# Kernel tuning notes

Hardware: AMD Instinct MI355X
Metric: run time of the kernel (lower is better)

Reference implementation:

```python
import jax, jax.numpy as jnp
import numpy as np
import math

H = 128      # hidden_channels
R = 32       # num_rbf
N = 4096     # atoms
E = 65536    # edges
CU = 4.5     # cutoff_upper (cutoff_lower = 0)
ALPHA = 5.0 / CU
MEANS = jnp.linspace(math.exp(-CU), 1.0, R, dtype=jnp.float32)
BETA = jnp.float32((2.0 / R * (1.0 - math.exp(-CU))) ** -2)
EPS = 1e-5


def _ln(x, g, b):
    mu = x.mean(-1, keepdims=True)
    var = ((x - mu) ** 2).mean(-1, keepdims=True)
    return (x - mu) * jax.lax.rsqrt(var + EPS) * g + b


def setup_inputs() -> dict:
    key = jax.random.key(0)
    ks = jax.random.split(key, 20)
    f32 = jnp.float32

    def w(i, shape):
        return jax.random.normal(ks[i], shape, f32) / np.float32(np.sqrt(shape[-1]))

    return {
        "edge_vec": jax.random.normal(ks[0], (E, 3), f32) * 1.5,
        "emb_w": w(1, (128, H)),
        "emb2_w": w(2, (H, 2 * H)), "emb2_b": jnp.zeros((H,), f32),
        "dp1_w": w(3, (H, R)), "dp1_b": jnp.zeros((H,), f32),
        "dp2_w": w(4, (H, R)), "dp2_b": jnp.zeros((H,), f32),
        "dp3_w": w(5, (H, R)), "dp3_b": jnp.zeros((H,), f32),
        "lt0_w": w(6, (H, H)), "lt1_w": w(7, (H, H)), "lt2_w": w(8, (H, H)),
        "ls0_w": w(9, (2 * H, H)), "ls0_b": jnp.zeros((2 * H,), f32),
        "ls1_w": w(10, (3 * H, 2 * H)), "ls1_b": jnp.zeros((3 * H,), f32),
        "init_g": jnp.ones((H,), f32), "init_b": jnp.zeros((H,), f32),
        "lin_w": w(11, (H, 3 * H)), "lin_b": jnp.zeros((H,), f32),
        "outn_g": jnp.ones((3 * H,), f32), "outn_b": jnp.zeros((3 * H,), f32),
        "ol1_w": w(12, (H // 2, H)), "ol1_b": jnp.zeros((H // 2,), f32),
        "ol2_w": w(13, (1, H // 2)), "ol2_b": jnp.zeros((1,), f32),
        "z": jax.random.randint(ks[14], (N,), 0, 128, dtype=jnp.int32),
        "edge_index": jax.random.randint(ks[15], (2, E), 0, N, dtype=jnp.int32),
    }


def reference(edge_vec, emb_w, emb2_w, emb2_b, dp1_w, dp1_b, dp2_w, dp2_b,
              dp3_w, dp3_b, lt0_w, lt1_w, lt2_w, ls0_w, ls0_b, ls1_w, ls1_b,
              init_g, init_b, lin_w, lin_b, outn_g, outn_b, ol1_w, ol1_b,
              ol2_w, ol2_b, z, edge_index):
    n = z.shape[0]
    src, dst = edge_index[0], edge_index[1]

    d = jnp.sqrt((edge_vec ** 2).sum(-1))                 # (E,)
    vn = edge_vec / d[:, None]                             # unit edge vectors
    cut = jnp.where(d < CU, 0.5 * (jnp.cos(jnp.pi * d / CU) + 1.0), 0.0)
    # expnorm RBF
    rbf = cut[:, None] * jnp.exp(-BETA * (jnp.exp(-ALPHA * d)[:, None] - MEANS) ** 2)  # (E,R)

    # atomic-number message Zij = emb2(cat(emb(z_i), emb(z_j)))
    zpair = jnp.concatenate([emb_w[z[src]], emb_w[z[dst]]], -1)  # (E,2H)
    zij = zpair @ emb2_w.T + emb2_b                              # (E,H)
    c = cut[:, None] * zij                                       # cutoff * Zij, (E,H)

    w1 = (rbf @ dp1_w.T + dp1_b) * c    # scalar channel weights (E,H)
    w2 = (rbf @ dp2_w.T + dp2_b) * c
    w3 = (rbf @ dp3_w.T + dp3_b) * c

    eye = jnp.eye(3, dtype=edge_vec.dtype)
    zero = jnp.zeros_like(vn[:, 0])
    skew = jnp.stack([zero, -vn[:, 2], vn[:, 1],
                      vn[:, 2], zero, -vn[:, 0],
                      -vn[:, 1], vn[:, 0], zero], 1).reshape(-1, 3, 3)  # (E,3,3)
    outer = vn[:, :, None] * vn[:, None, :]
    sym = outer - ((vn ** 2).sum(-1) / 3.0)[:, None, None] * eye        # traceless sym (E,3,3)

    seg = lambda a: jax.ops.segment_sum(a, src, num_segments=n)
    I0 = seg(w1)[:, :, None, None] * eye                                # (N,H,3,3)
    A0 = seg(w2[:, :, None, None] * skew[:, None, :, :])                # (N,H,3,3)
    S0 = seg(w3[:, :, None, None] * sym[:, None, :, :])                 # (N,H,3,3)

    tn = ((I0 + A0 + S0) ** 2).sum((-2, -1))                            # tensor_norm, (N,H)
    nrm = _ln(tn, init_g, init_b)
    h = jax.nn.silu(nrm @ ls0_w.T + ls0_b)
    scal = jax.nn.silu(h @ ls1_w.T + ls1_b).reshape(n, H, 3)            # per-channel gates

    I1 = jnp.einsum('nhxy,gh->ngxy', I0, lt0_w) * scal[..., 0][..., None, None]
    A1 = jnp.einsum('nhxy,gh->ngxy', A0, lt1_w) * scal[..., 1][..., None, None]
    S1 = jnp.einsum('nhxy,gh->ngxy', S0, lt2_w) * scal[..., 2][..., None, None]

    x = jnp.concatenate([(I1 ** 2).sum((-2, -1)),
                         (A1 ** 2).sum((-2, -1)),
                         (S1 ** 2).sum((-2, -1))], -1)                  # (N,3H)
    x = _ln(x, outn_g, outn_b)
    s1 = x @ lin_w.T + lin_b
    s2 = jax.nn.silu(s1) @ ol1_w.T + ol1_b
    s3 = jax.nn.silu(s2) @ ol2_w.T + ol2_b                              # per-atom energy (N,1)
    return s3
```

## Files before the change

kernel.cpp:

```cpp
#include <hip/hip_runtime.h>
#include <math.h>

#define NH_TOT 524288
#define N_ATOM 4096
#define N_EDGE 65536

typedef __attribute__((ext_vector_type(8))) short bf16x8;
typedef __attribute__((ext_vector_type(4))) float f32x4;

__device__ __forceinline__ unsigned short f2bf(float f) {
    unsigned u = __builtin_bit_cast(unsigned, f);
    unsigned r = (u + 0x7fffu + ((u >> 16) & 1u)) >> 16;
    return (unsigned short)r;
}
__device__ __forceinline__ float bf2f(unsigned short s) {
    unsigned u = ((unsigned)s) << 16;
    return __builtin_bit_cast(float, u);
}
__device__ __forceinline__ float silu(float v) { return v / (1.0f + __expf(-v)); }

#define WB_LS1 32768
#define WB_LT0 131072
#define WB_LT1 147456
#define WB_LT2 163840
#define WB_DP  180224

__global__ __launch_bounds__(256) void k_setup(
    const float* __restrict__ emb_w, const float* __restrict__ emb2_w,
    const int* __restrict__ ei, const int* __restrict__ z,
    const float* __restrict__ ls0_w, const float* __restrict__ ls1_w,
    const float* __restrict__ lt0_w, const float* __restrict__ lt1_w,
    const float* __restrict__ lt2_w,
    const float* __restrict__ dp1_w, const float* __restrict__ dp2_w,
    const float* __restrict__ dp3_w,
    float* __restrict__ U1, float* __restrict__ U2,
    int* __restrict__ cursor, int* __restrict__ order_pad,
    unsigned short* __restrict__ wb) {
    const int bx = blockIdx.x, tid = threadIdx.x;
    if (bx < 4096) {
        const int idx = bx * 4 + (tid >> 6);
        const int t = idx >> 7, h = idx & 127;
        const int lane = tid & 63;
        const float e0 = emb_w[t * 128 + lane];
        const float e1 = emb_w[t * 128 + 64 + lane];
        const float* row = emb2_w + h * 256;
        const float w0 = row[lane], w1 = row[64 + lane];
        const float w2 = row[128 + lane], w3 = row[192 + lane];
        float u1 = e0 * w0 + e1 * w1;
        float u2 = e0 * w2 + e1 * w3;
#pragma unroll
        for (int o = 1; o < 64; o <<= 1) {
            u1 += __shfl_xor(u1, o, 64);
            u2 += __shfl_xor(u2, o, 64);
        }
        if (lane == 0) {
            U1[t * 128 + h] = u1;
            U2[t * 128 + h] = u2;
        }
    } else if (bx < 4352) {
        const int e = (bx - 4096) * 256 + tid;
        const int src = ei[e];
        const int zd = z[ei[N_EDGE + e]];
        const int pos = atomicAdd(&cursor[src], 1);
        if (pos < 64) order_pad[(src << 6) + pos] = e | (zd << 16);
    } else {
        const int base = (bx - 4352) * 1024 + tid * 4;
        const float* src;
        int off;
        if (base < 32768)       { src = ls0_w; off = 0; }
        else if (base < 131072) { src = ls1_w; off = 32768; }
        else if (base < 147456) { src = lt0_w; off = 131072; }
        else if (base < 163840) { src = lt1_w; off = 147456; }
        else if (base < 180224) { src = lt2_w; off = 163840; }
        else if (base < 184320) { src = dp1_w; off = 180224; }
        else if (base < 188416) { src = dp2_w; off = 184320; }
        else                    { src = dp3_w; off = 188416; }
        const float4 v = *(const float4*)(src + (base - off));
        unsigned short* o = wb + base;
        o[0] = f2bf(v.x); o[1] = f2bf(v.y); o[2] = f2bf(v.z); o[3] = f2bf(v.w);
    }
}

__global__ __launch_bounds__(256) void k_fused(
    const int* __restrict__ z, const int* __restrict__ ecnt,
    const int* __restrict__ order_pad,
    const float* __restrict__ edge_vec,
    const float* __restrict__ U1, const float* __restrict__ U2,
    const float* __restrict__ emb2_b,
    const float* __restrict__ dp1_b, const float* __restrict__ dp2_b,
    const float* __restrict__ dp3_b,
    const unsigned short* __restrict__ wb,
    const float* __restrict__ init_g, const float* __restrict__ init_b,
    const float* __restrict__ ls0_b, const float* __restrict__ ls1_b,
    const float* __restrict__ outn_g, const float* __restrict__ outn_b,
    const float* __restrict__ lin_w, const float* __restrict__ lin_b,
    const float* __restrict__ ol1_w, const float* __restrict__ ol1_b,
    const float* __restrict__ ol2_w, const float* __restrict__ ol2_b,
    float* __restrict__ out) {
    const int tid = threadIdx.x;
    const int wave = tid >> 6, lane = tid & 63, lm = lane & 15, lq = lane >> 4;
    const int n0 = blockIdx.x * 8;
    const int ar = (lm < 8) ? lm : 7;

    __shared__ alignas(16) char smem[38912];
    unsigned short (*accs)[8][136] = reinterpret_cast<unsigned short(*)[8][136]>(smem);
    unsigned short (*nrms)[136]    = reinterpret_cast<unsigned short(*)[136]>(smem + 21760);
    unsigned short (*h1)[264]      = reinterpret_cast<unsigned short(*)[264]>(smem + 23936);
    unsigned short (*scal_s)[392]  = reinterpret_cast<unsigned short(*)[392]>(smem + 32384);
    float (*redS)[4]               = reinterpret_cast<float(*)[4]>(smem + 38656);
    float (*redQ)[4]               = reinterpret_cast<float(*)[4]>(smem + 38784);
    float (*xs)[392]               = reinterpret_cast<float(*)[392]>(smem);
    float (*ss)[132]               = reinterpret_cast<float(*)[132]>(smem + 23936);

    const unsigned short* dpw = wb + WB_DP;
    bf16x8 bfr[3][2];
    float bhc[2], bk1[2], bk2[2], bk3[2];
    int cols[2];
#pragma unroll
    for (int t = 0; t < 2; t++) {
        const int col = wave * 32 + t * 16 + lm;
        cols[t] = col;
        bhc[t] = emb2_b[col];
        bk1[t] = dp1_b[col]; bk2[t] = dp2_b[col]; bk3[t] = dp3_b[col];
#pragma unroll
        for (int k = 0; k < 3; k++)
            bfr[k][t] = *(const bf16x8*)(dpw + k * 4096 + col * 32 + lq * 8);
    }

    const float m0 = 0.011108996538242306f;
    const float dm = (1.0f - m0) * (1.0f / 31.0f);
    const float tb = 0.0625f * (1.0f - m0);
    const float beta = 1.0f / (tb * tb);
    const float mean0 = m0 + (float)(lq * 8) * dm;

    float tnA[8], tnB[8];

    for (int nn = 0; nn < 8; nn++) {
        const int n = n0 + nn;
        const int En = min(ecnt[n], 64);
        const int beg = n << 6;
        const int zoff = z[n] << 7;
        const float u1c0 = U1[zoff + cols[0]];
        const float u1c1 = U1[zoff + cols[1]];

        float part[10][2];
#pragma unroll
        for (int p = 0; p < 10; p++) { part[p][0] = 0.f; part[p][1] = 0.f; }

        for (int mi = 0; mi < En; mi += 16) {
            const int wrd = order_pad[beg + min(mi + lm, En - 1)];
            const int e = wrd & 0xFFFF;
            const int u2o = (wrd >> 16) << 7;
            const float evx = edge_vec[3 * e + 0];
            const float evy = edge_vec[3 * e + 1];
            const float evz = edge_vec[3 * e + 2];
            const float d = sqrtf(evx * evx + evy * evy + evz * evz);
            const float inv = 1.0f / d;
            const float cut = (d < 4.5f) ? 0.5f * (__cosf(0.6981317007977318f * d) + 1.0f) : 0.0f;
            const float vx = evx * inv, vy = evy * inv, vz = evz * inv;
            const float expd = __expf(-1.1111111111111112f * d);

            union { bf16x8 v; unsigned short s[8]; } uf;
#pragma unroll
            for (int j = 0; j < 8; j++) {
                const float df = expd - (mean0 + (float)j * dm);
                uf.s[j] = f2bf(cut * __expf(-beta * df * df));
            }
            const bf16x8 af = uf.v;

            f32x4 c[3][2];
#pragma unroll
            for (int k = 0; k < 3; k++)
#pragma unroll
                for (int t = 0; t < 2; t++)
                    c[k][t] = __builtin_amdgcn_mfma_f32_16x16x32_bf16(
                        af, bfr[k][t], (f32x4){0.f, 0.f, 0.f, 0.f}, 0, 0, 0);

#pragma unroll
            for (int r = 0; r < 4; r++) {
                const int er = mi + lq * 4 + r;
                const bool valid = er < En;
                const int sl = (lane & 48) | (lq * 4 + r);
                const float gvx = __shfl(vx, sl, 64);
                const float gvy = __shfl(vy, sl, 64);
                const float gvz = __shfl(vz, sl, 64);
                const float gct = __shfl(cut, sl, 64);
                const int   go  = __shfl(u2o, sl, 64);
#pragma unroll
                for (int t = 0; t < 2; t++) {
                    const float u2v = U2[go + cols[t]];
                    const float u1h = (t == 0) ? u1c0 : u1c1;
                    const float cc = valid ? gct * (u1h + u2v + bhc[t]) : 0.f;
                    const float w1 = (c[0][t][r] + bk1[t]) * cc;
                    const float w2 = (c[1][t][r] + bk2[t]) * cc;
                    const float w3 = (c[2][t][r] + bk3[t]) * cc;
                    part[0][t] += w1;
                    part[1][t] += w2 * gvx; part[2][t] += w2 * gvy; part[3][t] += w2 * gvz;
                    const float tx = w3 * gvx, ty = w3 * gvy;
                    part[4][t] += tx * gvx; part[5][t] += tx * gvy; part[6][t] += tx * gvz;
                    part[7][t] += ty * gvy; part[8][t] += ty * gvz; part[9][t] += w3 * gvz * gvz;
                }
            }
        }

#pragma unroll
        for (int p = 0; p < 10; p++)
#pragma unroll
            for (int t = 0; t < 2; t++) {
                float v = part[p][t];
                v += __shfl_xor(v, 16, 64);
                v += __shfl_xor(v, 32, 64);
                part[p][t] = v;
            }
        if (lq == 0) {
#pragma unroll
            for (int p = 0; p < 10; p++)
#pragma unroll
                for (int t = 0; t < 2; t++)
                    accs[p][nn][cols[t]] = f2bf(part[p][t]);
        }

        float tn[2];
#pragma unroll
        for (int t = 0; t < 2; t++) {
            const float aI = part[0][t];
            const float axv = part[1][t], ayv = part[2][t], azv = part[3][t];
            const float mxx = part[4][t], mxy = part[5][t], mxz = part[6][t];
            const float myy = part[7][t], myz = part[8][t], mzz = part[9][t];
            const float tr3 = (mxx + myy + mzz) * (1.0f / 3.0f);
            const float t00 = aI + mxx - tr3;
            const float t11 = aI + myy - tr3;
            const float t22 = aI + mzz - tr3;
            tn[t] = t00 * t00 + t11 * t11 + t22 * t22 +
                    2.0f * (mxy * mxy + azv * azv + mxz * mxz + ayv * ayv + myz * myz + axv * axv);
        }
        tnA[nn] = tn[0];
        tnB[nn] = tn[1];

        float s = (lq == 0) ? (tn[0] + tn[1]) : 0.f;
        s += __shfl_xor(s, 1, 64);
        s += __shfl_xor(s, 2, 64);
        s += __shfl_xor(s, 4, 64);
        s += __shfl_xor(s, 8, 64);
        if (lane == 0) redS[nn][wave] = s;
    }
    __syncthreads();

    {
        float dvA[8], dvB[8];
#pragma unroll
        for (int nn = 0; nn < 8; nn++) {
            const float mu = (redS[nn][0] + redS[nn][1] + redS[nn][2] + redS[nn][3]) * (1.0f / 128.0f);
            dvA[nn] = tnA[nn] - mu;
            dvB[nn] = tnB[nn] - mu;
            float q = (lq == 0) ? (dvA[nn] * dvA[nn] + dvB[nn] * dvB[nn]) : 0.f;
            q += __shfl_xor(q, 1, 64);
            q += __shfl_xor(q, 2, 64);
            q += __shfl_xor(q, 4, 64);
            q += __shfl_xor(q, 8, 64);
            if (lane == 0) redQ[nn][wave] = q;
        }
        __syncthreads();
        if (lq == 0) {
            const float g0 = init_g[cols[0]], g1 = init_g[cols[1]];
            const float b0 = init_b[cols[0]], b1 = init_b[cols[1]];
#pragma unroll
            for (int nn = 0; nn < 8; nn++) {
                const float var = (redQ[nn][0] + redQ[nn][1] + redQ[nn][2] + redQ[nn][3]) * (1.0f / 128.0f);
                const float rs = rsqrtf(var + 1e-5f);
                nrms[nn][cols[0]] = f2bf(dvA[nn] * rs * g0 + b0);
                nrms[nn][cols[1]] = f2bf(dvB[nn] * rs * g1 + b1);
            }
        }
    }
    __syncthreads();

    {
        f32x4 acc[4];
#pragma unroll
        for (int j = 0; j < 4; j++) acc[j] = (f32x4){0.f, 0.f, 0.f, 0.f};
        const int cbase = wave * 64;
#pragma unroll
        for (int kc = 0; kc < 128; kc += 32) {
            const bf16x8 af = *(const bf16x8*)(&nrms[ar][kc + lq * 8]);
#pragma unroll
            for (int sn = 0; sn < 4; sn++) {
                const bf16x8 b = *(const bf16x8*)(wb + (size_t)(cbase + sn * 16 + lm) * 128 + kc + lq * 8);
                acc[sn] = __builtin_amdgcn_mfma_f32_16x16x32_bf16(af, b, acc[sn], 0, 0, 0);
            }
        }
#pragma unroll
        for (int sn = 0; sn < 4; sn++) {
            const int col = cbase + sn * 16 + lm;
            const float bv = ls0_b[col];
#pragma unroll
            for (int r = 0; r < 4; r++)
                h1[lq * 4 + r][col] = f2bf(silu(acc[sn][r] + bv));
        }
    }
    __syncthreads();
    {
        f32x4 acc[6];
#pragma unroll
        for (int j = 0; j < 6; j++) acc[j] = (f32x4){0.f, 0.f, 0.f, 0.f};
        const int cbase = wave * 96;
        const unsigned short* ls1p = wb + WB_LS1;
#pragma unroll 2
        for (int kc = 0; kc < 256; kc += 32) {
            const bf16x8 af = *(const bf16x8*)(&h1[lm][kc + lq * 8]);
#pragma unroll
            for (int sn = 0; sn < 6; sn++) {
                const bf16x8 b = *(const bf16x8*)(ls1p + (size_t)(cbase + sn * 16 + lm) * 256 + kc + lq * 8);
                acc[sn] = __builtin_amdgcn_mfma_f32_16x16x32_bf16(af, b, acc[sn], 0, 0, 0);
            }
        }
#pragma unroll
        for (int sn = 0; sn < 6; sn++) {
            const int col = cbase + sn * 16 + lm;
            const float bv = ls1_b[col];
#pragma unroll
            for (int r = 0; r < 4; r++) {
                const int node = lq * 4 + r;
                if (node < 8) scal_s[node][col] = f2bf(silu(acc[sn][r] + bv));
            }
        }
    }
    __syncthreads();

    f32x4 e0[2], e1[2], e2[2], trv[2];
#pragma unroll
    for (int sn = 0; sn < 2; sn++) {
        e0[sn] = (f32x4){0.f, 0.f, 0.f, 0.f};
        e1[sn] = (f32x4){0.f, 0.f, 0.f, 0.f};
        e2[sn] = (f32x4){0.f, 0.f, 0.f, 0.f};
        trv[sn] = (f32x4){0.f, 0.f, 0.f, 0.f};
    }
#pragma unroll
    for (int p = 0; p < 10; p++) {
        const unsigned short* B = wb + (p == 0 ? WB_LT0 : (p < 4 ? WB_LT1 : WB_LT2));
        f32x4 c[2];
        c[0] = (f32x4){0.f, 0.f, 0.f, 0.f};
        c[1] = (f32x4){0.f, 0.f, 0.f, 0.f};
#pragma unroll
        for (int kc = 0; kc < 128; kc += 32) {
            const bf16x8 af = *(const bf16x8*)(&accs[p][ar][kc + lq * 8]);
#pragma unroll
            for (int sn = 0; sn < 2; sn++) {
                const bf16x8 b = *(const bf16x8*)(B + (size_t)(wave * 32 + sn * 16 + lm) * 128 + kc + lq * 8);
                c[sn] = __builtin_amdgcn_mfma_f32_16x16x32_bf16(af, b, c[sn], 0, 0, 0);
            }
        }
#pragma unroll
        for (int sn = 0; sn < 2; sn++) {
            if (p == 0)      e0[sn] += c[sn] * c[sn];
            else if (p < 4)  e1[sn] += c[sn] * c[sn];
            else if (p == 4 || p == 7 || p == 9) { e2[sn] += c[sn] * c[sn]; trv[sn] += c[sn]; }
            else             e2[sn] += 2.0f * c[sn] * c[sn];
        }
    }
    __syncthreads();

    if (lq < 2) {
#pragma unroll
        for (int sn = 0; sn < 2; sn++) {
            const int g = wave * 32 + sn * 16 + lm;
#pragma unroll
            for (int r = 0; r < 4; r++) {
                const int node = lq * 4 + r;
                const float s0 = bf2f(scal_s[node][3 * g + 0]);
                const float s1 = bf2f(scal_s[node][3 * g + 1]);
                const float s2 = bf2f(scal_s[node][3 * g + 2]);
                xs[node][g]       = 3.0f * e0[sn][r] * s0 * s0;
                xs[node][128 + g] = 2.0f * e1[sn][r] * s1 * s1;
                const float tr = trv[sn][r];
                xs[node][256 + g] = (e2[sn][r] - tr * tr * (1.0f / 3.0f)) * s2 * s2;
            }
        }
    }
    __syncthreads();

#pragma unroll
    for (int i = 0; i < 2; i++) {
        const int node = wave * 2 + i;
        float v[6];
        float s = 0.f;
#pragma unroll
        for (int j = 0; j < 6; j++) { v[j] = xs[node][lane + 64 * j]; s += v[j]; }
#pragma unroll
        for (int o = 1; o < 64; o <<= 1) s += __shfl_xor(s, o, 64);
        const float mu = s * (1.0f / 384.0f);
        float q = 0.f;
#pragma unroll
        for (int j = 0; j < 6; j++) { v[j] -= mu; q += v[j] * v[j]; }
#pragma unroll
        for (int o = 1; o < 64; o <<= 1) q += __shfl_xor(q, o, 64);
        const float rs = rsqrtf(q * (1.0f / 384.0f) + 1e-5f);
#pragma unroll
        for (int j = 0; j < 6; j++) {
            const int col = lane + 64 * j;
            xs[node][col] = v[j] * rs * outn_g[col] + outn_b[col];
        }
    }
    __syncthreads();

    {
        const int j = tid & 127, half = tid >> 7;
        float a4[4];
        const float lb = lin_b[j];
#pragma unroll
        for (int i = 0; i < 4; i++) a4[i] = lb;
        const float4* wr = (const float4*)(lin_w + j * 384);
#pragma unroll 2
        for (int k4 = 0; k4 < 96; k4++) {
            const float4 w4 = wr[k4];
#pragma unroll
            for (int i = 0; i < 4; i++) {
                const float4 xv = *(const float4*)&xs[half * 4 + i][k4 * 4];
                a4[i] += w4.x * xv.x + w4.y * xv.y + w4.z * xv.z + w4.w * xv.w;
            }
        }
        __syncthreads();
#pragma unroll
        for (int i = 0; i < 4; i++) ss[half * 4 + i][j] = silu(a4[i]);
    }
    __syncthreads();

    {
        const int o = tid & 63, q = tid >> 6;
        float a2v[2];
        const float ob = ol1_b[o];
        a2v[0] = ob; a2v[1] = ob;
        const float4* o4 = (const float4*)(ol1_w + o * 128);
#pragma unroll 4
        for (int k4 = 0; k4 < 32; k4++) {
            const float4 w4 = o4[k4];
#pragma unroll
            for (int i = 0; i < 2; i++) {
                const float4 sv = *(const float4*)&ss[q * 2 + i][k4 * 4];
                a2v[i] += w4.x * sv.x + w4.y * sv.y + w4.z * sv.z + w4.w * sv.w;
            }
        }
        const float w2 = ol2_w[o];
#pragma unroll
        for (int i = 0; i < 2; i++) {
            float v = silu(a2v[i]) * w2;
            for (int s = 32; s > 0; s >>= 1) v += __shfl_down(v, s, 64);
            if (o == 0) out[n0 + q * 2 + i] = v + ol2_b[0];
        }
    }
}

extern "C" void kernel_launch(void* const* d_in, const int* in_sizes, int n_in,
                              void* d_out, int out_size, void* d_ws, size_t ws_size,
                              hipStream_t stream) {
    (void)in_sizes; (void)n_in; (void)out_size; (void)ws_size;
    const float* edge_vec = (const float*)d_in[0];
    const float* emb_w   = (const float*)d_in[1];
    const float* emb2_w  = (const float*)d_in[2];
    const float* emb2_b  = (const float*)d_in[3];
    const float* dp1_w   = (const float*)d_in[4];
    const float* dp1_b   = (const float*)d_in[5];
    const float* dp2_w   = (const float*)d_in[6];
    const float* dp2_b   = (const float*)d_in[7];
    const float* dp3_w   = (const float*)d_in[8];
    const float* dp3_b   = (const float*)d_in[9];
    const float* lt0_w   = (const float*)d_in[10];
    const float* lt1_w   = (const float*)d_in[11];
    const float* lt2_w   = (const float*)d_in[12];
    const float* ls0_w   = (const float*)d_in[13];
    const float* ls0_b   = (const float*)d_in[14];
    const float* ls1_w   = (const float*)d_in[15];
    const float* ls1_b   = (const float*)d_in[16];
    const float* init_g  = (const float*)d_in[17];
    const float* init_b  = (const float*)d_in[18];
    const float* lin_w   = (const float*)d_in[19];
    const float* lin_b   = (const float*)d_in[20];
    const float* outn_g  = (const float*)d_in[21];
    const float* outn_b  = (const float*)d_in[22];
    const float* ol1_w   = (const float*)d_in[23];
    const float* ol1_b   = (const float*)d_in[24];
    const float* ol2_w   = (const float*)d_in[25];
    const float* ol2_b   = (const float*)d_in[26];
    const int* z  = (const int*)d_in[27];
    const int* ei = (const int*)d_in[28];
    float* out = (float*)d_out;

    char* w = (char*)d_ws;
    int*            cursor    = (int*)(w);
    unsigned short* wb        = (unsigned short*)(w + 16384);
    float*          U1        = (float*)(w + 401408);
    float*          U2        = (float*)(w + 466944);
    int*            order_pad = (int*)(w + 532480);

    hipMemsetAsync(w, 0, 16384, stream);
    k_setup<<<dim3(4540), dim3(256), 0, stream>>>(emb_w, emb2_w, ei, z,
                                                  ls0_w, ls1_w, lt0_w, lt1_w, lt2_w,
                                                  dp1_w, dp2_w, dp3_w,
                                                  U1, U2, cursor, order_pad, wb);
    k_fused<<<dim3(512), dim3(256), 0, stream>>>(z, cursor, order_pad, edge_vec,
                                                 U1, U2, emb2_b, dp1_b, dp2_b, dp3_b, wb,
                                                 init_g, init_b, ls0_b, ls1_b,
                                                 outn_g, outn_b, lin_w, lin_b,
                                                 ol1_w, ol1_b, ol2_w, ol2_b, out);
}
```

Baseline: 212.0 us.

## Double block to 512 threads, splitting atoms and tensor components across two wave teams

The fused kernel now runs 8 waves per block instead of 4, grouped into two teams of 4. Each team handles 4 of the block's 8 atoms in the edge-accumulation phase and half of the 10 tensor components in the lt-matmul phase. Partial e2/trace sums are exchanged through shared memory. The MLP stages are re-split so each wave does less work. This raises per-block parallelism and latency hiding on a grid of only 512 blocks, at the cost of an extra exchange barrier and possibly lower occupancy if register use stays high under launch_bounds(512).

Measured after the change: 257.2 us. 21.3% more time.

```diff
diff --git a/kernel.cpp b/kernel.cpp
--- a/kernel.cpp
+++ b/kernel.cpp
@@ -81,7 +81,7 @@
     }
 }
 
-__global__ __launch_bounds__(256) void k_fused(
+__global__ __launch_bounds__(512) void k_fused(
     const int* __restrict__ z, const int* __restrict__ ecnt,
     const int* __restrict__ order_pad,
     const float* __restrict__ edge_vec,
@@ -99,6 +99,7 @@
     float* __restrict__ out) {
     const int tid = threadIdx.x;
     const int wave = tid >> 6, lane = tid & 63, lm = lane & 15, lq = lane >> 4;
+    const int team = wave >> 2, tw = wave & 3;
     const int n0 = blockIdx.x * 8;
     const int ar = (lm < 8) ? lm : 7;
 
@@ -111,6 +112,7 @@
     float (*redQ)[4]               = reinterpret_cast<float(*)[4]>(smem + 38784);
     float (*xs)[392]               = reinterpret_cast<float(*)[392]>(smem);
     float (*ss)[132]               = reinterpret_cast<float(*)[132]>(smem + 23936);
+    float* exch                    = reinterpret_cast<float*>(smem + 23936);
 
     const unsigned short* dpw = wb + WB_DP;
     bf16x8 bfr[3][2];
@@ -118,7 +120,7 @@
     int cols[2];
 #pragma unroll
     for (int t = 0; t < 2; t++) {
-        const int col = wave * 32 + t * 16 + lm;
+        const int col = tw * 32 + t * 16 + lm;
         cols[t] = col;
         bhc[t] = emb2_b[col];
         bk1[t] = dp1_b[col]; bk2[t] = dp2_b[col]; bk3[t] = dp3_b[col];
@@ -133,9 +135,10 @@
     const float beta = 1.0f / (tb * tb);
     const float mean0 = m0 + (float)(lq * 8) * dm;
 
-    float tnA[8], tnB[8];
-
-    for (int nn = 0; nn < 8; nn++) {
+    float tnA[4], tnB[4];
+
+    for (int nn2 = 0; nn2 < 4; nn2++) {
+        const int nn = team * 4 + nn2;
         const int n = n0 + nn;
         const int En = min(ecnt[n], 64);
         const int beg = n << 6;
@@ -234,88 +237,90 @@
             tn[t] = t00 * t00 + t11 * t11 + t22 * t22 +
                     2.0f * (mxy * mxy + azv * azv + mxz * mxz + ayv * ayv + myz * myz + axv * axv);
         }
-        tnA[nn] = tn[0];
-        tnB[nn] = tn[1];
+        tnA[nn2] = tn[0];
+        tnB[nn2] = tn[1];
 
         float s = (lq == 0) ? (tn[0] + tn[1]) : 0.f;
         s += __shfl_xor(s, 1, 64);
         s += __shfl_xor(s, 2, 64);
         s += __shfl_xor(s, 4, 64);
         s += __shfl_xor(s, 8, 64);
-        if (lane == 0) redS[nn][wave] = s;
+        if (lane == 0) redS[nn][tw] = s;
     }
     __syncthreads();
 
     {
-        float dvA[8], dvB[8];
-#pragma unroll
-        for (int nn = 0; nn < 8; nn++) {
+        float dvA[4], dvB[4];
+#pragma unroll
+        for (int nn2 = 0; nn2 < 4; nn2++) {
+            const int nn = team * 4 + nn2;
             const float mu = (redS[nn][0] + redS[nn][1] + redS[nn][2] + redS[nn][3]) * (1.0f / 128.0f);
-            dvA[nn] = tnA[nn] - mu;
-            dvB[nn] = tnB[nn] - mu;
-            float q = (lq == 0) ? (dvA[nn] * dvA[nn] + dvB[nn] * dvB[nn]) : 0.f;
+            dvA[nn2] = tnA[nn2] - mu;
+            dvB[nn2] = tnB[nn2] - mu;
+            float q = (lq == 0) ? (dvA[nn2] * dvA[nn2] + dvB[nn2] * dvB[nn2]) : 0.f;
             q += __shfl_xor(q, 1, 64);
             q += __shfl_xor(q, 2, 64);
             q += __shfl_xor(q, 4, 64);
             q += __shfl_xor(q, 8, 64);
-            if (lane == 0) redQ[nn][wave] = q;
+            if (lane == 0) redQ[nn][tw] = q;
         }
         __syncthreads();
         if (lq == 0) {
             const float g0 = init_g[cols[0]], g1 = init_g[cols[1]];
             const float b0 = init_b[cols[0]], b1 = init_b[cols[1]];
 #pragma unroll
-            for (int nn = 0; nn < 8; nn++) {
+            for (int nn2 = 0; nn2 < 4; nn2++) {
+                const int nn = team * 4 + nn2;
                 const float var = (redQ[nn][0] + redQ[nn][1] + redQ[nn][2] + redQ[nn][3]) * (1.0f / 128.0f);
                 const float rs = rsqrtf(var + 1e-5f);
-                nrms[nn][cols[0]] = f2bf(dvA[nn] * rs * g0 + b0);
-                nrms[nn][cols[1]] = f2bf(dvB[nn] * rs * g1 + b1);
+                nrms[nn][cols[0]] = f2bf(dvA[nn2] * rs * g0 + b0);
+                nrms[nn][cols[1]] = f2bf(dvB[nn2] * rs * g1 + b1);
             }
         }
     }
     __syncthreads();
 
     {
+        f32x4 acc[2];
+        acc[0] = (f32x4){0.f, 0.f, 0.f, 0.f};
+        acc[1] = (f32x4){0.f, 0.f, 0.f, 0.f};
+        const int cbase = wave * 32;
+#pragma unroll
+        for (int kc = 0; kc < 128; kc += 32) {
+            const bf16x8 af = *(const bf16x8*)(&nrms[ar][kc + lq * 8]);
+#pragma unroll
+            for (int sn = 0; sn < 2; sn++) {
+                const bf16x8 b = *(const bf16x8*)(wb + (size_t)(cbase + sn * 16 + lm) * 128 + kc + lq * 8);
+                acc[sn] = __builtin_amdgcn_mfma_f32_16x16x32_bf16(af, b, acc[sn], 0, 0, 0);
+            }
+        }
+#pragma unroll
+        for (int sn = 0; sn < 2; sn++) {
+            const int col = cbase + sn * 16 + lm;
+            const float bv = ls0_b[col];
+#pragma unroll
+            for (int r = 0; r < 4; r++)
+                h1[lq * 4 + r][col] = f2bf(silu(acc[sn][r] + bv));
+        }
+    }
+    __syncthreads();
+    if (wave < 6) {
         f32x4 acc[4];
 #pragma unroll
         for (int j = 0; j < 4; j++) acc[j] = (f32x4){0.f, 0.f, 0.f, 0.f};
         const int cbase = wave * 64;
-#pragma unroll
-        for (int kc = 0; kc < 128; kc += 32) {
-            const bf16x8 af = *(const bf16x8*)(&nrms[ar][kc + lq * 8]);
-#pragma unroll
-            for (int sn = 0; sn < 4; sn++) {
-                const bf16x8 b = *(const bf16x8*)(wb + (size_t)(cbase + sn * 16 + lm) * 128 + kc + lq * 8);
-                acc[sn] = __builtin_amdgcn_mfma_f32_16x16x32_bf16(af, b, acc[sn], 0, 0, 0);
-            }
-        }
-#pragma unroll
-        for (int sn = 0; sn < 4; sn++) {
-            const int col = cbase + sn * 16 + lm;
-            const float bv = ls0_b[col];
-#pragma unroll
-            for (int r = 0; r < 4; r++)
-                h1[lq * 4 + r][col] = f2bf(silu(acc[sn][r] + bv));
-        }
-    }
-    __syncthreads();
-    {
-        f32x4 acc[6];
-#pragma unroll
-        for (int j = 0; j < 6; j++) acc[j] = (f32x4){0.f, 0.f, 0.f, 0.f};
-        const int cbase = wave * 96;
         const unsigned short* ls1p = wb + WB_LS1;
 #pragma unroll 2
         for (int kc = 0; kc < 256; kc += 32) {
             const bf16x8 af = *(const bf16x8*)(&h1[lm][kc + lq * 8]);
 #pragma unroll
-            for (int sn = 0; sn < 6; sn++) {
+            for (int sn = 0; sn < 4; sn++) {
                 const bf16x8 b = *(const bf16x8*)(ls1p + (size_t)(cbase + sn * 16 + lm) * 256 + kc + lq * 8);
                 acc[sn] = __builtin_amdgcn_mfma_f32_16x16x32_bf16(af, b, acc[sn], 0, 0, 0);
             }
         }
 #pragma unroll
-        for (int sn = 0; sn < 6; sn++) {
+        for (int sn = 0; sn < 4; sn++) {
             const int col = cbase + sn * 16 + lm;
             const float bv = ls1_b[col];
 #pragma unroll
@@ -336,7 +341,8 @@
         trv[sn] = (f32x4){0.f, 0.f, 0.f, 0.f};
     }
 #pragma unroll
-    for (int p = 0; p < 10; p++) {
+    for (int pp = 0; pp < 5; pp++) {
+        const int p = team * 5 + pp;
         const unsigned short* B = wb + (p == 0 ? WB_LT0 : (p < 4 ? WB_LT1 : WB_LT2));
         f32x4 c[2];
         c[0] = (f32x4){0.f, 0.f, 0.f, 0.f};
@@ -346,7 +352,7 @@
             const bf16x8 af = *(const bf16x8*)(&accs[p][ar][kc + lq * 8]);
 #pragma unroll
             for (int sn = 0; sn < 2; sn++) {
-                const bf16x8 b = *(const bf16x8*)(B + (size_t)(wave * 32 + sn * 16 + lm) * 128 + kc + lq * 8);
+                const bf16x8 b = *(const bf16x8*)(B + (size_t)(tw * 32 + sn * 16 + lm) * 128 + kc + lq * 8);
                 c[sn] = __builtin_amdgcn_mfma_f32_16x16x32_bf16(af, b, c[sn], 0, 0, 0);
             }
         }
@@ -360,28 +366,42 @@
     }
     __syncthreads();
 
-    if (lq < 2) {
-#pragma unroll
-        for (int sn = 0; sn < 2; sn++) {
-            const int g = wave * 32 + sn * 16 + lm;
+    if (team == 1 && lq < 2) {
+#pragma unroll
+        for (int sn = 0; sn < 2; sn++)
 #pragma unroll
             for (int r = 0; r < 4; r++) {
                 const int node = lq * 4 + r;
+                const int idx = ((tw * 2 + sn) * 8 + node) * 16 + lm;
+                exch[idx] = e2[sn][r];
+                exch[1024 + idx] = trv[sn][r];
+            }
+    }
+    __syncthreads();
+
+    if (team == 0 && lq < 2) {
+#pragma unroll
+        for (int sn = 0; sn < 2; sn++) {
+#pragma unroll
+            for (int r = 0; r < 4; r++) {
+                const int node = lq * 4 + r;
+                const int g = tw * 32 + sn * 16 + lm;
+                const int idx = ((tw * 2 + sn) * 8 + node) * 16 + lm;
+                const float e2t = e2[sn][r] + exch[idx];
+                const float trt = trv[sn][r] + exch[1024 + idx];
                 const float s0 = bf2f(scal_s[node][3 * g + 0]);
                 const float s1 = bf2f(scal_s[node][3 * g + 1]);
                 const float s2 = bf2f(scal_s[node][3 * g + 2]);
                 xs[node][g]       = 3.0f * e0[sn][r] * s0 * s0;
                 xs[node][128 + g] = 2.0f * e1[sn][r] * s1 * s1;
-                const float tr = trv[sn][r];
-                xs[node][256 + g] = (e2[sn][r] - tr * tr * (1.0f / 3.0f)) * s2 * s2;
-            }
-        }
-    }
-    __syncthreads();
-
-#pragma unroll
-    for (int i = 0; i < 2; i++) {
-        const int node = wave * 2 + i;
+                xs[node][256 + g] = (e2t - trt * trt * (1.0f / 3.0f)) * s2 * s2;
+            }
+        }
+    }
+    __syncthreads();
+
+    {
+        const int node = wave;
         float v[6];
         float s = 0.f;
 #pragma unroll
@@ -404,49 +424,39 @@
     __syncthreads();
 
     {
-        const int j = tid & 127, half = tid >> 7;
-        float a4[4];
+        const int j = tid & 127, grp = tid >> 7;
+        float a2[2];
         const float lb = lin_b[j];
-#pragma unroll
-        for (int i = 0; i < 4; i++) a4[i] = lb;
+        a2[0] = lb; a2[1] = lb;
         const float4* wr = (const float4*)(lin_w + j * 384);
 #pragma unroll 2
         for (int k4 = 0; k4 < 96; k4++) {
             const float4 w4 = wr[k4];
 #pragma unroll
-            for (int i = 0; i < 4; i++) {
-                const float4 xv = *(const float4*)&xs[half * 4 + i][k4 * 4];
-                a4[i] += w4.x * xv.x + w4.y * xv.y + w4.z * xv.z + w4.w * xv.w;
+            for (int i = 0; i < 2; i++) {
+                const float4 xv = *(const float4*)&xs[grp * 2 + i][k4 * 4];
+                a2[i] += w4.x * xv.x + w4.y * xv.y + w4.z * xv.z + w4.w * xv.w;
             }
         }
         __syncthreads();
 #pragma unroll
-        for (int i = 0; i < 4; i++) ss[half * 4 + i][j] = silu(a4[i]);
+        for (int i = 0; i < 2; i++) ss[grp * 2 + i][j] = silu(a2[i]);
     }
     __syncthreads();
 
     {
         const int o = tid & 63, q = tid >> 6;
-        float a2v[2];
-        const float ob = ol1_b[o];
-        a2v[0] = ob; a2v[1] = ob;
+        float a = ol1_b[o];
         const float4* o4 = (const float4*)(ol1_w + o * 128);
 #pragma unroll 4
         for (int k4 = 0; k4 < 32; k4++) {
             const float4 w4 = o4[k4];
-#pragma unroll
-            for (int i = 0; i < 2; i++) {
-                const float4 sv = *(const float4*)&ss[q * 2 + i][k4 * 4];
-                a2v[i] += w4.x * sv.x + w4.y * sv.y + w4.z * sv.z + w4.w * sv.w;
-            }
-        }
-        const float w2 = ol2_w[o];
-#pragma unroll
-        for (int i = 0; i < 2; i++) {
-            float v = silu(a2v[i]) * w2;
-            for (int s = 32; s > 0; s >>= 1) v += __shfl_down(v, s, 64);
-            if (o == 0) out[n0 + q * 2 + i] = v + ol2_b[0];
-        }
+            const float4 sv = *(const float4*)&ss[q][k4 * 4];
+            a += w4.x * sv.x + w4.y * sv.y + w4.z * sv.z + w4.w * sv.w;
+        }
+        float v = silu(a) * ol2_w[o];
+        for (int s = 32; s > 0; s >>= 1) v += __shfl_down(v, s, 64);
+        if (o == 0) out[n0 + q] = v + ol2_b[0];
     }
 }
 
@@ -497,7 +507,7 @@
                                                   ls0_w, ls1_w, lt0_w, lt1_w, lt2_w,
                                                   dp1_w, dp2_w, dp3_w,
                                                   U1, U2, cursor, order_pad, wb);
-    k_fused<<<dim3(512), dim3(256), 0, stream>>>(z, cursor, order_pad, edge_vec,
+    k_fused<<<dim3(512), dim3(512), 0, stream>>>(z, cursor, order_pad, edge_vec,
                                                  U1, U2, emb2_b, dp1_b, dp2_b, dp3_b, wb,
                                                  init_g, init_b, ls0_b, ls1_b,
                                                  outn_g, outn_b, lin_w, lin_b,
```
